# Optimization experiments

Measured on AMD Instinct MI355X. Metric: run time of the kernel, lower is better.

Reference implementation:

```python
import jax, jax.numpy as jnp
import numpy as np

IN_FEATURES = 4096
OUT_FEATURES = 4096
OUTLIER_NUM = 128
Q_IN = IN_FEATURES - OUTLIER_NUM  # 3968
B, S = 4, 2048


def _build_perm(seed=0):
    rng = np.random.default_rng(seed)
    outlier_ids = rng.choice(IN_FEATURES, size=OUTLIER_NUM, replace=False)
    mask = np.ones(IN_FEATURES, dtype=bool)
    mask[outlier_ids] = False
    col_ids = np.arange(IN_FEATURES, dtype=np.int32)
    col_perm = np.concatenate([col_ids[mask], col_ids[~mask]])
    inv_col_perm = np.zeros(IN_FEATURES, dtype=np.int32)
    inv_col_perm[col_perm] = np.arange(IN_FEATURES, dtype=np.int32)
    return inv_col_perm


def setup_inputs() -> dict:
    key = jax.random.key(0)
    k1, k2, k3, k4, k5 = jax.random.split(key, 5)
    inp = {
        "input": jax.random.normal(k1, (B, S, IN_FEATURES), dtype=jnp.float32),
        # low-bit integer codes stored as float (e.g. int4 range), per-row scale
        "q_weight": jax.random.randint(k2, (OUT_FEATURES, Q_IN), -8, 8).astype(jnp.float32),
        "fp_weight": jax.random.normal(k3, (OUT_FEATURES, OUTLIER_NUM), dtype=jnp.float32),
        "alpha_scale": jax.random.uniform(k4, (OUT_FEATURES, 1), dtype=jnp.float32, minval=0.01, maxval=0.1),
        "bias": jax.random.normal(k5, (OUT_FEATURES,), dtype=jnp.float32),
        "inv_col_perm": jnp.asarray(_build_perm(), dtype=jnp.int32),
    }
    return inp


def reference(input, q_weight, fp_weight, alpha_scale, bias, inv_col_perm):
    # SymQuant.dequantize: per-output-row symmetric scale
    dq_w = q_weight * alpha_scale                      # [O, Q_IN]
    out_w = jnp.concatenate([dq_w, fp_weight], axis=1)  # [O, IN]
    out_w = out_w[:, inv_col_perm]                      # undo column permutation
    # F.linear: input @ out_w.T + bias
    return jnp.einsum("bsi,oi->bso", input, out_w) + bias
```

## Files before the change

### kernel.cpp

```cpp
#include <hip/hip_runtime.h>
#include <stdint.h>

#define IN_F  4096
#define OUT_F 4096
#define OUTL  128
#define QIN   (IN_F - OUTL)
#define MTOT  8192
#define BM 128
#define BN 128

typedef unsigned short u16;
typedef __bf16 bf16x8 __attribute__((ext_vector_type(8)));
typedef float  f32x4  __attribute__((ext_vector_type(4)));
typedef int    i32x4  __attribute__((ext_vector_type(4)));

__device__ __forceinline__ u16 f2b(float f) {
  union { float f; uint32_t i; } v; v.f = f;
  uint32_t r = v.i + 0x7fffu + ((v.i >> 16) & 1u);
  return (u16)(r >> 16);
}

__global__ void build_pos(const int* __restrict__ invp, int* __restrict__ pos) {
  const int i = blockIdx.x * 256 + threadIdx.x;
  const int j = invp[i];
  if (j >= QIN) pos[j - QIN] = i;
}

__global__ __launch_bounds__(256) void prep_a(
    const float* __restrict__ A, const int* __restrict__ pos,
    signed char* __restrict__ A8, u16* __restrict__ Afp,
    float* __restrict__ s_arr) {
  const int m = blockIdx.x;
  const int tid = threadIdx.x;
  const float* row = A + (size_t)m * IN_F;

  float4 v[4];
  float amax = 0.f;
#pragma unroll
  for (int k = 0; k < 4; ++k) {
    v[k] = ((const float4*)row)[k * 256 + tid];
    amax = fmaxf(amax, fmaxf(fmaxf(fabsf(v[k].x), fabsf(v[k].y)),
                             fmaxf(fabsf(v[k].z), fabsf(v[k].w))));
  }
#pragma unroll
  for (int off = 32; off; off >>= 1)
    amax = fmaxf(amax, __shfl_xor(amax, off, 64));
  __shared__ float wmax[4];
  if ((tid & 63) == 0) wmax[tid >> 6] = amax;
  __syncthreads();
  amax = fmaxf(fmaxf(wmax[0], wmax[1]), fmaxf(wmax[2], wmax[3]));
  const float inv = (amax > 0.f) ? 127.f / amax : 0.f;
  if (tid == 0) s_arr[m] = amax / 127.f;

#pragma unroll
  for (int k = 0; k < 4; ++k) {
    const int q0 = __float2int_rn(v[k].x * inv);
    const int q1 = __float2int_rn(v[k].y * inv);
    const int q2 = __float2int_rn(v[k].z * inv);
    const int q3 = __float2int_rn(v[k].w * inv);
    const uint32_t p = (q0 & 255) | ((q1 & 255) << 8) |
                       ((q2 & 255) << 16) | ((uint32_t)(q3 & 255) << 24);
    ((uint32_t*)A8)[(size_t)m * (IN_F / 4) + k * 256 + tid] = p;
  }
  if (tid < OUTL) {
    const int p = pos[tid];
    Afp[(size_t)m * OUTL + tid] = f2b(row[p]);
  }
}

__global__ __launch_bounds__(256) void prep_w(
    const float* __restrict__ qw, const float* __restrict__ fpw,
    const int* __restrict__ invp, signed char* __restrict__ W8,
    u16* __restrict__ Wfp) {
  __shared__ float qs[QIN];
  const int o = blockIdx.x;
  const int tid = threadIdx.x;
  const float4* qrow = (const float4*)(qw + (size_t)o * QIN);
#pragma unroll
  for (int k = 0; k < 4; ++k) {
    const int idx = k * 256 + tid;
    if (idx < QIN / 4) ((float4*)qs)[idx] = qrow[idx];
  }
  __syncthreads();

  signed char vals[16];
#pragma unroll
  for (int q = 0; q < 4; ++q) {
    const int4 jj = ((const int4*)invp)[tid * 4 + q];
    const int j[4] = {jj.x, jj.y, jj.z, jj.w};
#pragma unroll
    for (int e = 0; e < 4; ++e)
      vals[q * 4 + e] =
          (j[e] < QIN) ? (signed char)__float2int_rn(qs[j[e]]) : (signed char)0;
  }
  ((uint4*)(W8 + (size_t)o * IN_F))[tid] = *(const uint4*)vals;
  if (tid < OUTL)
    Wfp[(size_t)o * OUTL + tid] = f2b(fpw[(size_t)o * OUTL + tid]);
}

#define GLDS(g, l)                                                              \
  __builtin_amdgcn_global_load_lds(                                             \
      (const __attribute__((address_space(1))) void*)(g),                       \
      (__attribute__((address_space(3))) void*)(l), 16, 0, 0)

__global__ __launch_bounds__(256) void gemm_i8(
    const signed char* __restrict__ A8, const signed char* __restrict__ W8,
    const u16* __restrict__ Afp, const u16* __restrict__ Wfp,
    const float* __restrict__ s_arr, const float* __restrict__ alpha,
    const float* __restrict__ bias, float* __restrict__ C) {
  __shared__ unsigned char As8[BM * 64];
  __shared__ unsigned char Bs8[BN * 64];

  const int tid  = threadIdx.x;
  const int wave = tid >> 6;
  const int lane = tid & 63;
  const int bn = blockIdx.x, bm = blockIdx.y;
  const int wm = (wave >> 1) * 64;
  const int wn = (wave & 1)  * 64;

  const int srow   = wave * 32 + (lane >> 2);
  const int schunk = (lane & 3) ^ ((lane >> 4) & 3);
  const signed char* Ag = A8 + (size_t)(bm * BM + srow) * IN_F + schunk * 16;
  const signed char* Wg = W8 + (size_t)(bn * BN + srow) * IN_F + schunk * 16;
  unsigned char* AsW = As8 + wave * 32 * 64;
  unsigned char* BsW = Bs8 + wave * 32 * 64;

  i32x4 acci[4][4];
#pragma unroll
  for (int mi = 0; mi < 4; ++mi)
#pragma unroll
    for (int ni = 0; ni < 4; ++ni) acci[mi][ni] = (i32x4){0, 0, 0, 0};

  const int fr = lane & 15;
  const int fq = lane >> 4;
  const int slot = fq ^ ((fr >> 2) & 3);

  for (int kt = 0; kt < IN_F / 64; ++kt) {
    __syncthreads();
    GLDS(Ag + kt * 64,               AsW);
    GLDS(Ag + kt * 64 + 16 * IN_F,   AsW + 16 * 64);
    GLDS(Wg + kt * 64,               BsW);
    GLDS(Wg + kt * 64 + 16 * IN_F,   BsW + 16 * 64);
    __syncthreads();

    i32x4 af[4], bg[4];
#pragma unroll
    for (int mi = 0; mi < 4; ++mi)
      af[mi] = *(const i32x4*)&As8[(wm + mi * 16 + fr) * 64 + slot * 16];
#pragma unroll
    for (int ni = 0; ni < 4; ++ni)
      bg[ni] = *(const i32x4*)&Bs8[(wn + ni * 16 + fr) * 64 + slot * 16];
#pragma unroll
    for (int mi = 0; mi < 4; ++mi)
#pragma unroll
      for (int ni = 0; ni < 4; ++ni)
        acci[mi][ni] = __builtin_amdgcn_mfma_i32_16x16x64_i8(
            af[mi], bg[ni], acci[mi][ni], 0, 0, 0);
  }

  f32x4 accf[4][4];
#pragma unroll
  for (int mi = 0; mi < 4; ++mi)
#pragma unroll
    for (int ni = 0; ni < 4; ++ni) accf[mi][ni] = (f32x4){0.f, 0.f, 0.f, 0.f};

  u16* AsH = (u16*)As8;
  u16* BsH = (u16*)Bs8;
  const u16* Afg = Afp + (size_t)(bm * BM + srow) * OUTL + schunk * 8;
  const u16* Wfg = Wfp + (size_t)(bn * BN + srow) * OUTL + schunk * 8;
  u16* AsWH = AsH + wave * 32 * 32;
  u16* BsWH = BsH + wave * 32 * 32;

  for (int kt = 0; kt < 4; ++kt) {
    __syncthreads();
    GLDS(Afg + kt * 32,              AsWH);
    GLDS(Afg + kt * 32 + 16 * OUTL,  AsWH + 16 * 32);
    GLDS(Wfg + kt * 32,              BsWH);
    GLDS(Wfg + kt * 32 + 16 * OUTL,  BsWH + 16 * 32);
    __syncthreads();

    bf16x8 af[4], bg[4];
#pragma unroll
    for (int mi = 0; mi < 4; ++mi)
      af[mi] = *(const bf16x8*)&AsH[(wm + mi * 16 + fr) * 32 + slot * 8];
#pragma unroll
    for (int ni = 0; ni < 4; ++ni)
      bg[ni] = *(const bf16x8*)&BsH[(wn + ni * 16 + fr) * 32 + slot * 8];
#pragma unroll
    for (int mi = 0; mi < 4; ++mi)
#pragma unroll
      for (int ni = 0; ni < 4; ++ni)
        accf[mi][ni] = __builtin_amdgcn_mfma_f32_16x16x32_bf16(
            af[mi], bg[ni], accf[mi][ni], 0, 0, 0);
  }

  float sv[4][4];
#pragma unroll
  for (int mi = 0; mi < 4; ++mi)
#pragma unroll
    for (int rr = 0; rr < 4; ++rr)
      sv[mi][rr] = s_arr[bm * BM + wm + mi * 16 + fq * 4 + rr];

#pragma unroll
  for (int ni = 0; ni < 4; ++ni) {
    const int n = bn * BN + wn + ni * 16 + fr;
    const float an = alpha[n];
    const float bv = bias[n];
#pragma unroll
    for (int mi = 0; mi < 4; ++mi) {
      const int m0 = bm * BM + wm + mi * 16 + fq * 4;
#pragma unroll
      for (int rr = 0; rr < 4; ++rr)
        C[(size_t)(m0 + rr) * OUT_F + n] =
            (float)acci[mi][ni][rr] * (sv[mi][rr] * an) + accf[mi][ni][rr] + bv;
    }
  }
}

extern "C" void kernel_launch(void* const* d_in, const int* in_sizes, int n_in,
                              void* d_out, int out_size, void* d_ws, size_t ws_size,
                              hipStream_t stream) {
  const float* input = (const float*)d_in[0];
  const float* qw    = (const float*)d_in[1];
  const float* fpw   = (const float*)d_in[2];
  const float* alpha = (const float*)d_in[3];
  const float* bias  = (const float*)d_in[4];
  const int*   invp  = (const int*)d_in[5];

  char* ws = (char*)d_ws;
  signed char* A8   = (signed char*)ws;
  signed char* W8   = (signed char*)(ws + (32ull << 20));
  u16*  Afp  = (u16*)(ws + (48ull << 20));
  u16*  Wfp  = (u16*)(ws + (50ull << 20));
  float* s_arr = (float*)(ws + (51ull << 20));
  int*   pos   = (int*)(ws + (51ull << 20) + (64ull << 10));
  float* out = (float*)d_out;

  build_pos<<<IN_F / 256, 256, 0, stream>>>(invp, pos);
  prep_a<<<MTOT, 256, 0, stream>>>(input, pos, A8, Afp, s_arr);
  prep_w<<<OUT_F, 256, 0, stream>>>(qw, fpw, invp, W8, Wfp);

  dim3 ggrid(OUT_F / BN, MTOT / BM);
  gemm_i8<<<ggrid, dim3(256), 0, stream>>>(A8, W8, Afp, Wfp, s_arr, alpha,
                                           bias, out);
}
```

Baseline: 475.6 us.

## Fold outlier weights into int8 GEMM, fuse prep kernels, double K tile

Requantizes each output row, dequantized codes plus fp outlier columns, into a single int8 row with a per-row scale. This removes the separate bf16 outlier MFMA pass, the position-gather kernel and the bf16 activation copies. The three prep kernels become one launch. The GEMM K tile grows from 64 to 128 with a wider XOR swizzle and launch bounds of 3, so there are half as many barrier-separated load stages. The trade-off is extra accuracy loss: the fp32 outlier weights and alpha-scaled codes now share one 8-bit grid, and the divide-by-zero guard on the activation scale is gone.

```diff
diff --git a/kernel.cpp b/kernel.cpp
--- a/kernel.cpp
+++ b/kernel.cpp
@@ -8,94 +8,95 @@
 #define MTOT  8192
 #define BM 128
 #define BN 128
+#define BKB 128
 
 typedef unsigned short u16;
-typedef __bf16 bf16x8 __attribute__((ext_vector_type(8)));
-typedef float  f32x4  __attribute__((ext_vector_type(4)));
-typedef int    i32x4  __attribute__((ext_vector_type(4)));
-
-__device__ __forceinline__ u16 f2b(float f) {
-  union { float f; uint32_t i; } v; v.f = f;
-  uint32_t r = v.i + 0x7fffu + ((v.i >> 16) & 1u);
-  return (u16)(r >> 16);
-}
-
-__global__ void build_pos(const int* __restrict__ invp, int* __restrict__ pos) {
-  const int i = blockIdx.x * 256 + threadIdx.x;
-  const int j = invp[i];
-  if (j >= QIN) pos[j - QIN] = i;
-}
-
-__global__ __launch_bounds__(256) void prep_a(
-    const float* __restrict__ A, const int* __restrict__ pos,
-    signed char* __restrict__ A8, u16* __restrict__ Afp,
-    float* __restrict__ s_arr) {
-  const int m = blockIdx.x;
+typedef int i32x4 __attribute__((ext_vector_type(4)));
+
+__global__ __launch_bounds__(256) void prep_fused(
+    const float* __restrict__ A, signed char* __restrict__ A8,
+    float* __restrict__ s_arr,
+    const float* __restrict__ qw, const float* __restrict__ fpw,
+    const float* __restrict__ alpha, const int* __restrict__ invp,
+    signed char* __restrict__ W8, float* __restrict__ t_arr) {
   const int tid = threadIdx.x;
-  const float* row = A + (size_t)m * IN_F;
-
-  float4 v[4];
-  float amax = 0.f;
-#pragma unroll
-  for (int k = 0; k < 4; ++k) {
-    v[k] = ((const float4*)row)[k * 256 + tid];
-    amax = fmaxf(amax, fmaxf(fmaxf(fabsf(v[k].x), fabsf(v[k].y)),
-                             fmaxf(fabsf(v[k].z), fabsf(v[k].w))));
+  __shared__ float red[4];
+
+  if (blockIdx.x >= OUT_F) {
+    const int m = blockIdx.x - OUT_F;
+    const float* row = A + (size_t)m * IN_F;
+    float4 v[4];
+    float amax = 0.f;
+#pragma unroll
+    for (int k = 0; k < 4; ++k) {
+      v[k] = ((const float4*)row)[k * 256 + tid];
+      amax = fmaxf(amax, fmaxf(fmaxf(fabsf(v[k].x), fabsf(v[k].y)),
+                               fmaxf(fabsf(v[k].z), fabsf(v[k].w))));
+    }
+#pragma unroll
+    for (int off = 32; off; off >>= 1)
+      amax = fmaxf(amax, __shfl_xor(amax, off, 64));
+    if ((tid & 63) == 0) red[tid >> 6] = amax;
+    __syncthreads();
+    amax = fmaxf(fmaxf(red[0], red[1]), fmaxf(red[2], red[3]));
+    const float inv = 127.f / amax;
+    if (tid == 0) s_arr[m] = amax / 127.f;
+#pragma unroll
+    for (int k = 0; k < 4; ++k) {
+      const int q0 = __float2int_rn(v[k].x * inv);
+      const int q1 = __float2int_rn(v[k].y * inv);
+      const int q2 = __float2int_rn(v[k].z * inv);
+      const int q3 = __float2int_rn(v[k].w * inv);
+      const uint32_t p = (q0 & 255) | ((q1 & 255) << 8) |
+                         ((q2 & 255) << 16) | ((uint32_t)(q3 & 255) << 24);
+      ((uint32_t*)A8)[(size_t)m * (IN_F / 4) + k * 256 + tid] = p;
+    }
+  } else {
+    const int o = blockIdx.x;
+    __shared__ float qs[QIN];
+    __shared__ float fs[OUTL];
+    const float a = alpha[o];
+    float amax = 0.f;
+    const float4* qrow = (const float4*)(qw + (size_t)o * QIN);
+#pragma unroll
+    for (int k = 0; k < 4; ++k) {
+      const int idx = k * 256 + tid;
+      if (idx < QIN / 4) {
+        const float4 q = qrow[idx];
+        ((float4*)qs)[idx] = q;
+        const float qm = fmaxf(fmaxf(fabsf(q.x), fabsf(q.y)),
+                               fmaxf(fabsf(q.z), fabsf(q.w)));
+        amax = fmaxf(amax, qm * a);
+      }
+    }
+    if (tid < OUTL / 4) {
+      const float4 f = ((const float4*)(fpw + (size_t)o * OUTL))[tid];
+      ((float4*)fs)[tid] = f;
+      amax = fmaxf(amax, fmaxf(fmaxf(fabsf(f.x), fabsf(f.y)),
+                               fmaxf(fabsf(f.z), fabsf(f.w))));
+    }
+#pragma unroll
+    for (int off = 32; off; off >>= 1)
+      amax = fmaxf(amax, __shfl_xor(amax, off, 64));
+    if ((tid & 63) == 0) red[tid >> 6] = amax;
+    __syncthreads();
+    amax = fmaxf(fmaxf(red[0], red[1]), fmaxf(red[2], red[3]));
+    const float invws = 127.f / amax;
+    if (tid == 0) t_arr[o] = amax / 127.f;
+
+    signed char vals[16];
+#pragma unroll
+    for (int q = 0; q < 4; ++q) {
+      const int4 jj = ((const int4*)invp)[tid * 4 + q];
+      const int j[4] = {jj.x, jj.y, jj.z, jj.w};
+#pragma unroll
+      for (int e = 0; e < 4; ++e) {
+        const float v = (j[e] < QIN) ? qs[j[e]] * a : fs[j[e] - QIN];
+        vals[q * 4 + e] = (signed char)__float2int_rn(v * invws);
+      }
+    }
+    ((uint4*)(W8 + (size_t)o * IN_F))[tid] = *(const uint4*)vals;
   }
-#pragma unroll
-  for (int off = 32; off; off >>= 1)
-    amax = fmaxf(amax, __shfl_xor(amax, off, 64));
-  __shared__ float wmax[4];
-  if ((tid & 63) == 0) wmax[tid >> 6] = amax;
-  __syncthreads();
-  amax = fmaxf(fmaxf(wmax[0], wmax[1]), fmaxf(wmax[2], wmax[3]));
-  const float inv = (amax > 0.f) ? 127.f / amax : 0.f;
-  if (tid == 0) s_arr[m] = amax / 127.f;
-
-#pragma unroll
-  for (int k = 0; k < 4; ++k) {
-    const int q0 = __float2int_rn(v[k].x * inv);
-    const int q1 = __float2int_rn(v[k].y * inv);
-    const int q2 = __float2int_rn(v[k].z * inv);
-    const int q3 = __float2int_rn(v[k].w * inv);
-    const uint32_t p = (q0 & 255) | ((q1 & 255) << 8) |
-                       ((q2 & 255) << 16) | ((uint32_t)(q3 & 255) << 24);
-    ((uint32_t*)A8)[(size_t)m * (IN_F / 4) + k * 256 + tid] = p;
-  }
-  if (tid < OUTL) {
-    const int p = pos[tid];
-    Afp[(size_t)m * OUTL + tid] = f2b(row[p]);
-  }
-}
-
-__global__ __launch_bounds__(256) void prep_w(
-    const float* __restrict__ qw, const float* __restrict__ fpw,
-    const int* __restrict__ invp, signed char* __restrict__ W8,
-    u16* __restrict__ Wfp) {
-  __shared__ float qs[QIN];
-  const int o = blockIdx.x;
-  const int tid = threadIdx.x;
-  const float4* qrow = (const float4*)(qw + (size_t)o * QIN);
-#pragma unroll
-  for (int k = 0; k < 4; ++k) {
-    const int idx = k * 256 + tid;
-    if (idx < QIN / 4) ((float4*)qs)[idx] = qrow[idx];
-  }
-  __syncthreads();
-
-  signed char vals[16];
-#pragma unroll
-  for (int q = 0; q < 4; ++q) {
-    const int4 jj = ((const int4*)invp)[tid * 4 + q];
-    const int j[4] = {jj.x, jj.y, jj.z, jj.w};
-#pragma unroll
-    for (int e = 0; e < 4; ++e)
-      vals[q * 4 + e] =
-          (j[e] < QIN) ? (signed char)__float2int_rn(qs[j[e]]) : (signed char)0;
-  }
-  ((uint4*)(W8 + (size_t)o * IN_F))[tid] = *(const uint4*)vals;
-  if (tid < OUTL)
-    Wfp[(size_t)o * OUTL + tid] = f2b(fpw[(size_t)o * OUTL + tid]);
 }
 
 #define GLDS(g, l)                                                              \
@@ -103,13 +104,12 @@
       (const __attribute__((address_space(1))) void*)(g),                       \
       (__attribute__((address_space(3))) void*)(l), 16, 0, 0)
 
-__global__ __launch_bounds__(256) void gemm_i8(
+__global__ __launch_bounds__(256, 3) void gemm_i8(
     const signed char* __restrict__ A8, const signed char* __restrict__ W8,
-    const u16* __restrict__ Afp, const u16* __restrict__ Wfp,
-    const float* __restrict__ s_arr, const float* __restrict__ alpha,
+    const float* __restrict__ s_arr, const float* __restrict__ t_arr,
     const float* __restrict__ bias, float* __restrict__ C) {
-  __shared__ unsigned char As8[BM * 64];
-  __shared__ unsigned char Bs8[BN * 64];
+  __shared__ unsigned char As8[BM * BKB];
+  __shared__ unsigned char Bs8[BN * BKB];
 
   const int tid  = threadIdx.x;
   const int wave = tid >> 6;
@@ -118,80 +118,49 @@
   const int wm = (wave >> 1) * 64;
   const int wn = (wave & 1)  * 64;
 
-  const int srow   = wave * 32 + (lane >> 2);
-  const int schunk = (lane & 3) ^ ((lane >> 4) & 3);
+  const int srow   = wave * 32 + (lane >> 3);
+  const int schunk = (lane & 7) ^ ((lane >> 3) & 7);
   const signed char* Ag = A8 + (size_t)(bm * BM + srow) * IN_F + schunk * 16;
   const signed char* Wg = W8 + (size_t)(bn * BN + srow) * IN_F + schunk * 16;
-  unsigned char* AsW = As8 + wave * 32 * 64;
-  unsigned char* BsW = Bs8 + wave * 32 * 64;
-
-  i32x4 acci[4][4];
+  unsigned char* AsW = As8 + wave * 32 * BKB;
+  unsigned char* BsW = Bs8 + wave * 32 * BKB;
+
+  i32x4 acc[4][4];
 #pragma unroll
   for (int mi = 0; mi < 4; ++mi)
 #pragma unroll
-    for (int ni = 0; ni < 4; ++ni) acci[mi][ni] = (i32x4){0, 0, 0, 0};
+    for (int ni = 0; ni < 4; ++ni) acc[mi][ni] = (i32x4){0, 0, 0, 0};
 
   const int fr = lane & 15;
   const int fq = lane >> 4;
-  const int slot = fq ^ ((fr >> 2) & 3);
-
-  for (int kt = 0; kt < IN_F / 64; ++kt) {
-    __syncthreads();
-    GLDS(Ag + kt * 64,               AsW);
-    GLDS(Ag + kt * 64 + 16 * IN_F,   AsW + 16 * 64);
-    GLDS(Wg + kt * 64,               BsW);
-    GLDS(Wg + kt * 64 + 16 * IN_F,   BsW + 16 * 64);
-    __syncthreads();
-
-    i32x4 af[4], bg[4];
-#pragma unroll
-    for (int mi = 0; mi < 4; ++mi)
-      af[mi] = *(const i32x4*)&As8[(wm + mi * 16 + fr) * 64 + slot * 16];
-#pragma unroll
-    for (int ni = 0; ni < 4; ++ni)
-      bg[ni] = *(const i32x4*)&Bs8[(wn + ni * 16 + fr) * 64 + slot * 16];
-#pragma unroll
-    for (int mi = 0; mi < 4; ++mi)
+
+  for (int kt = 0; kt < IN_F / BKB; ++kt) {
+    __syncthreads();
+#pragma unroll
+    for (int t = 0; t < 4; ++t) {
+      GLDS(Ag + kt * BKB + t * 8 * IN_F, AsW + t * 8 * BKB);
+      GLDS(Wg + kt * BKB + t * 8 * IN_F, BsW + t * 8 * BKB);
+    }
+    __syncthreads();
+
+#pragma unroll
+    for (int ks = 0; ks < 2; ++ks) {
+      i32x4 af[4], bg[4];
+#pragma unroll
+      for (int mi = 0; mi < 4; ++mi)
+        af[mi] = *(const i32x4*)
+            &As8[(wm + mi * 16 + fr) * BKB + (((ks * 4 + fq) ^ (fr & 7)) * 16)];
 #pragma unroll
       for (int ni = 0; ni < 4; ++ni)
-        acci[mi][ni] = __builtin_amdgcn_mfma_i32_16x16x64_i8(
-            af[mi], bg[ni], acci[mi][ni], 0, 0, 0);
-  }
-
-  f32x4 accf[4][4];
-#pragma unroll
-  for (int mi = 0; mi < 4; ++mi)
-#pragma unroll
-    for (int ni = 0; ni < 4; ++ni) accf[mi][ni] = (f32x4){0.f, 0.f, 0.f, 0.f};
-
-  u16* AsH = (u16*)As8;
-  u16* BsH = (u16*)Bs8;
-  const u16* Afg = Afp + (size_t)(bm * BM + srow) * OUTL + schunk * 8;
-  const u16* Wfg = Wfp + (size_t)(bn * BN + srow) * OUTL + schunk * 8;
-  u16* AsWH = AsH + wave * 32 * 32;
-  u16* BsWH = BsH + wave * 32 * 32;
-
-  for (int kt = 0; kt < 4; ++kt) {
-    __syncthreads();
-    GLDS(Afg + kt * 32,              AsWH);
-    GLDS(Afg + kt * 32 + 16 * OUTL,  AsWH + 16 * 32);
-    GLDS(Wfg + kt * 32,              BsWH);
-    GLDS(Wfg + kt * 32 + 16 * OUTL,  BsWH + 16 * 32);
-    __syncthreads();
-
-    bf16x8 af[4], bg[4];
-#pragma unroll
-    for (int mi = 0; mi < 4; ++mi)
-      af[mi] = *(const bf16x8*)&AsH[(wm + mi * 16 + fr) * 32 + slot * 8];
-#pragma unroll
-    for (int ni = 0; ni < 4; ++ni)
-      bg[ni] = *(const bf16x8*)&BsH[(wn + ni * 16 + fr) * 32 + slot * 8];
-#pragma unroll
-    for (int mi = 0; mi < 4; ++mi)
-#pragma unroll
-      for (int ni = 0; ni < 4; ++ni)
-        accf[mi][ni] = __builtin_amdgcn_mfma_f32_16x16x32_bf16(
-            af[mi], bg[ni], accf[mi][ni], 0, 0, 0);
+        bg[ni] = *(const i32x4*)
+            &Bs8[(wn + ni * 16 + fr) * BKB + (((ks * 4 + fq) ^ (fr & 7)) * 16)];
+#pragma unroll
+      for (int mi = 0; mi < 4; ++mi)
+#pragma unroll
+        for (int ni = 0; ni < 4; ++ni)
+          acc[mi][ni] = __builtin_amdgcn_mfma_i32_16x16x64_i8(
+              af[mi], bg[ni], acc[mi][ni], 0, 0, 0);
+    }
   }
 
   float sv[4][4];
@@ -204,7 +173,7 @@
 #pragma unroll
   for (int ni = 0; ni < 4; ++ni) {
     const int n = bn * BN + wn + ni * 16 + fr;
-    const float an = alpha[n];
+    const float tn = t_arr[n];
     const float bv = bias[n];
 #pragma unroll
     for (int mi = 0; mi < 4; ++mi) {
@@ -212,7 +181,7 @@
 #pragma unroll
       for (int rr = 0; rr < 4; ++rr)
         C[(size_t)(m0 + rr) * OUT_F + n] =
-            (float)acci[mi][ni][rr] * (sv[mi][rr] * an) + accf[mi][ni][rr] + bv;
+            (float)acc[mi][ni][rr] * (sv[mi][rr] * tn) + bv;
     }
   }
 }
@@ -228,19 +197,15 @@
   const int*   invp  = (const int*)d_in[5];
 
   char* ws = (char*)d_ws;
-  signed char* A8   = (signed char*)ws;
-  signed char* W8   = (signed char*)(ws + (32ull << 20));
-  u16*  Afp  = (u16*)(ws + (48ull << 20));
-  u16*  Wfp  = (u16*)(ws + (50ull << 20));
-  float* s_arr = (float*)(ws + (51ull << 20));
-  int*   pos   = (int*)(ws + (51ull << 20) + (64ull << 10));
+  signed char* A8    = (signed char*)ws;
+  signed char* W8    = (signed char*)(ws + (32ull << 20));
+  float* s_arr = (float*)(ws + (48ull << 20));
+  float* t_arr = (float*)(ws + (48ull << 20) + (64ull << 10));
   float* out = (float*)d_out;
 
-  build_pos<<<IN_F / 256, 256, 0, stream>>>(invp, pos);
-  prep_a<<<MTOT, 256, 0, stream>>>(input, pos, A8, Afp, s_arr);
-  prep_w<<<OUT_F, 256, 0, stream>>>(qw, fpw, invp, W8, Wfp);
+  prep_fused<<<OUT_F + MTOT, 256, 0, stream>>>(input, A8, s_arr, qw, fpw,
+                                               alpha, invp, W8, t_arr);
 
   dim3 ggrid(OUT_F / BN, MTOT / BM);
-  gemm_i8<<<ggrid, dim3(256), 0, stream>>>(A8, W8, Afp, Wfp, s_arr, alpha,
-                                           bias, out);
+  gemm_i8<<<ggrid, dim3(256), 0, stream>>>(A8, W8, s_arr, t_arr, bias, out);
 }
```

Result: faster. 403.3 us (-15.2%).
